# Kernel optimization log

Measured on AMD Instinct MI355X. Metric: run time of the kernel, lower is better.

Reference implementation:

```python
import jax, jax.numpy as jnp
import numpy as np


def _hard_sigmoid(x):
    # Keras ConvLSTM2D default recurrent_activation
    return jnp.clip(0.2 * x + 0.5, 0.0, 1.0)


def _conv(x, w):
    # NHWC input, HWIO kernel, SAME padding, stride 1
    return jax.lax.conv_general_dilated(
        x, w, (1, 1), 'SAME', dimension_numbers=('NHWC', 'HWIO', 'NHWC'))


def _convlstm(seq, h, c, k, rk, b):
    # seq: [B, T, H, W, Cin]; h, c: [B, H, W, F]
    # k: [kh, kw, Cin, 4F], rk: [kh, kw, F, 4F], b: [4F]
    def step(carry, x):
        h, c = carry
        z = _conv(x, k) + _conv(h, rk) + b  # [B,H,W,4F]
        zi, zf, zc, zo = jnp.split(z, 4, axis=-1)
        i = _hard_sigmoid(zi)
        f = _hard_sigmoid(zf)
        o = _hard_sigmoid(zo)
        c = f * c + i * jnp.tanh(zc)
        h = o * jnp.tanh(c)
        return (h, c), None
    (h, c), _ = jax.lax.scan(step, (h, c), jnp.swapaxes(seq, 0, 1))
    return h, c


def setup_inputs() -> dict:
    key = jax.random.key(0)
    ks = jax.random.split(key, 14)
    B, T, H, W, Cin, F, K = 32, 1, 64, 64, 1, 64, 3
    s = 0.05
    inp = {
        'input_': jax.random.normal(ks[0], (B, T, H, W, Cin), jnp.float32),
        'h0': jax.random.normal(ks[1], (B, H, W, F), jnp.float32) * s,
        'c0': jax.random.normal(ks[2], (B, H, W, F), jnp.float32) * s,
        'h1': jax.random.normal(ks[3], (B, H, W, F), jnp.float32) * s,
        'c1': jax.random.normal(ks[4], (B, H, W, F), jnp.float32) * s,
        'k0': jax.random.normal(ks[5], (K, K, Cin, 4 * F), jnp.float32) * s,
        'rk0': jax.random.normal(ks[6], (K, K, F, 4 * F), jnp.float32) * s,
        'b0': jnp.zeros((4 * F,), jnp.float32),
        'k1': jax.random.normal(ks[7], (K, K, F, 4 * F), jnp.float32) * s,
        'rk1': jax.random.normal(ks[8], (K, K, F, 4 * F), jnp.float32) * s,
        'b1': jnp.zeros((4 * F,), jnp.float32),
        'cw': jax.random.normal(ks[9], (1, 1, F, 1), jnp.float32) * s,
        'cb': jnp.zeros((1,), jnp.float32),
    }
    return inp


def reference(input_, h0, c0, h1, c1, k0, rk0, b0, k1, rk1, b1, cw, cb):
    # Layer 0 consumes the input frame sequence (T=1)
    h0n, c0n = _convlstm(input_, h0, c0, k0, rk0, b0)
    # Layer 1 consumes layer-0's last hidden state as its (length-1) input
    h1n, c1n = _convlstm(h0n[:, None], h1, c1, k1, rk1, b1)
    frames = _conv(h1n, cw) + cb  # 1x1 conv head -> [B,H,W,1]
    return frames, h0n, c0n, h1n, c1n
```

## Files before the change

kernel.cpp:

```cpp
#include <hip/hip_runtime.h>
#include <hip/hip_bf16.h>

typedef short s16;
typedef __attribute__((ext_vector_type(8))) short bf16x8;
typedef __attribute__((ext_vector_type(4))) float f32x4;

__device__ __forceinline__ s16 f2bf(float f) {
  unsigned u = __builtin_bit_cast(unsigned, f);
  unsigned r = (u + 0x7FFFu + ((u >> 16) & 1u)) >> 16;
  return (s16)r;
}

__device__ __forceinline__ float hsig(float x) {
  return fminf(fmaxf(0.2f * x + 0.5f, 0.0f), 1.0f);
}

#define PXS 66
#define ROWSZ (PXS * 64)
#define ASZ4 (4 * ROWSZ)
#define ASZ6 (6 * ROWSZ)

__global__ void wprep_kernel(const float* __restrict__ rk0, const float* __restrict__ k1,
                             const float* __restrict__ rk1, const float* __restrict__ k0,
                             s16* __restrict__ w0q, s16* __restrict__ w1q,
                             s16* __restrict__ w2q, s16* __restrict__ k0t) {
  int idx = blockIdx.x * 256 + threadIdx.x;
  const int n1 = 18 * 8192;
  if (idx < 3 * n1) {
    int which = idx / n1;
    int i = idx - which * n1;
    int e    = i & 7;
    int lane = (i >> 3) & 63;
    int g    = (i >> 9) & 3;
    int j    = (i >> 11) & 3;
    int k    = (i >> 13) & 1;
    int tap  = i >> 14;
    int l15 = lane & 15, l4 = lane >> 4;
    int ic = k * 32 + l4 * 8 + e;
    int oc = j * 64 + g * 16 + l15;
    const float* src = (which == 0) ? rk0 : (which == 1) ? k1 : rk1;
    s16* dst = (which == 0) ? w0q : (which == 1) ? w1q : w2q;
    dst[i] = f2bf(src[(tap * 64 + ic) * 256 + oc]);
  } else if (idx < 3 * n1 + 8192) {
    int r = idx - 3 * n1;
    int kk = r & 31;
    int oc = r >> 5;
    k0t[r] = (kk < 9) ? f2bf(k0[kk * 256 + oc]) : (s16)0;
  }
}

template <bool F32>
__device__ __forceinline__ bf16x8 load_conv8(const void* src, long off) {
  if constexpr (F32) {
    const float* p = (const float*)src + off;
    float4 v0 = *reinterpret_cast<const float4*>(p);
    float4 v1 = *reinterpret_cast<const float4*>(p + 4);
    bf16x8 r;
    r[0] = f2bf(v0.x); r[1] = f2bf(v0.y); r[2] = f2bf(v0.z); r[3] = f2bf(v0.w);
    r[4] = f2bf(v1.x); r[5] = f2bf(v1.y); r[6] = f2bf(v1.z); r[7] = f2bf(v1.w);
    return r;
  } else {
    return *reinterpret_cast<const bf16x8*>((const s16*)src + off);
  }
}

template <bool F32, int ROWS, int NT>
__device__ __forceinline__ void stageA(s16* a_lds, const void* src, int b, int y0, int tid) {
  #pragma unroll
  for (int i = 0; i < ROWS * 512 / NT; ++i) {
    int c   = tid + i * NT;
    int row = c >> 9;
    int px  = (c >> 3) & 63;
    int cb  = c & 7;
    int y   = y0 - 1 + row;
    int xp  = px + 1;
    bf16x8 v = {};
    if ((unsigned)y < 64u)
      v = load_conv8<F32>(src, ((long)(b * 64 + y) * 64 + px) * 64 + cb * 8);
    *reinterpret_cast<bf16x8*>(a_lds + (row * PXS + xp) * 64 + ((cb ^ (xp & 7)) * 8)) = v;
  }
  if (tid < ROWS * 16) {
    int row = tid >> 4;
    int xp  = ((tid >> 3) & 1) ? 65 : 0;
    int cb  = tid & 7;
    bf16x8 z = {};
    *reinterpret_cast<bf16x8*>(a_lds + (row * PXS + xp) * 64 + cb * 8) = z;
  }
}

__global__ __launch_bounds__(1024, 1) void cell0_kernel(
    const float* __restrict__ h0,
    const s16* __restrict__ w0,
    const float* __restrict__ xin,
    const s16* __restrict__ k0t,
    const float* __restrict__ bias,
    const float* __restrict__ c_old,
    float* __restrict__ h_out,
    float* __restrict__ c_out,
    s16* __restrict__ hb_out)
{
  __shared__ __align__(16) s16 a_lds[ASZ6];
  __shared__ __align__(16) s16 w_lds[3][8192];
  __shared__ float x_lds[384];

  const int tid = threadIdx.x;
  const int b  = blockIdx.x >> 4;
  const int y0 = (blockIdx.x & 15) << 2;

  const int wave = tid >> 6;
  const int lane = tid & 63;
  const int g    = wave & 3;
  const int mh   = wave >> 2;
  const int l15  = lane & 15;
  const int l4   = lane >> 4;

  constexpr int NST = 18;

  auto issueW = [&](int u) {
    int v = (u >= NST) ? u - NST : u;
    const s16* wt = w0 + v * 8192;
    char* base = (char*)(&w_lds[0][0]) + (v % 3) * 16384 + (tid >> 6) * 1024;
    __builtin_amdgcn_global_load_lds(
        (const __attribute__((address_space(1))) void*)(wt + tid * 8),
        (__attribute__((address_space(3))) void*)base, 16, 0, 0);
  };
  auto readWf = [&](bf16x8 (&wf)[4], int slot) {
    const s16* wb = &w_lds[slot][0] + g * 512 + lane * 8;
    #pragma unroll
    for (int j = 0; j < 4; ++j)
      wf[j] = *reinterpret_cast<const bf16x8*>(wb + j * 2048);
  };

  f32x4 acc[4][4] = {};

  auto doStage = [&](const bf16x8 (&wf)[4], int u) {
    int tap = u >> 1, kk = u & 1;
    int dy = tap / 3, dx = tap - dy * 3;
    const char* sb = (const char*)a_lds + (mh + dy) * (ROWSZ * 2);
    bf16x8 af[4];
    #pragma unroll
    for (int m = 0; m < 4; ++m) {
      int xq   = m * 16 + l15 + dx;
      int boff = xq * 128 + ((((kk << 2) | l4) ^ (xq & 7)) << 4);
      af[m] = *reinterpret_cast<const bf16x8*>(sb + boff);
    }
    __builtin_amdgcn_s_setprio(1);
    #pragma unroll
    for (int m = 0; m < 4; ++m) {
      #pragma unroll
      for (int j = 0; j < 4; ++j)
        acc[m][j] = __builtin_amdgcn_mfma_f32_16x16x32_bf16(af[m], wf[j], acc[m][j], 0, 0, 0);
    }
    __builtin_amdgcn_s_setprio(0);
  };

  issueW(0);
  issueW(1);
  stageA<true, 6, 1024>(a_lds, h0, b, y0, tid);
  if (tid < 384) {
    int row = tid >> 6, px = tid & 63;
    int y = y0 - 1 + row;
    x_lds[tid] = ((unsigned)y < 64u) ? xin[(b * 64 + y) * 64 + px] : 0.0f;
  }
  __syncthreads();

  {
    bf16x8 bx[4];
    #pragma unroll
    for (int j = 0; j < 4; ++j) {
      int oc = j * 64 + g * 16 + l15;
      bx[j] = *reinterpret_cast<const bf16x8*>(k0t + oc * 32 + l4 * 8);
    }
    #pragma unroll
    for (int m = 0; m < 4; ++m) {
      int px = m * 16 + l15;
      bf16x8 ax = {};
      #pragma unroll
      for (int e = 0; e < 8; ++e) {
        int t = l4 * 8 + e;
        if (t < 9) {
          int dyt = t / 3, dxt = t - dyt * 3;
          int xx = px + dxt - 1;
          float xv = ((unsigned)xx < 64u) ? x_lds[(mh + dyt) * 64 + xx] : 0.0f;
          ax[e] = f2bf(xv);
        }
      }
      #pragma unroll
      for (int j = 0; j < 4; ++j)
        acc[m][j] = __builtin_amdgcn_mfma_f32_16x16x32_bf16(ax, bx[j], acc[m][j], 0, 0, 0);
    }
  }

  bf16x8 wf[4];
  #pragma unroll
  for (int u = 0; u < NST; ++u) {
    asm volatile("s_waitcnt vmcnt(1)" ::: "memory");
    __builtin_amdgcn_s_barrier();
    __builtin_amdgcn_sched_barrier(0);
    issueW(u + 2);
    readWf(wf, u % 3);
    doStage(wf, u);
  }

  float bi[4];
  #pragma unroll
  for (int j = 0; j < 4; ++j) bi[j] = bias[j * 64 + g * 16 + l15];
  const int pix_base = b * 4096 + y0 * 64;
  const int f = g * 16 + l15;
  #pragma unroll
  for (int m = 0; m < 4; ++m) {
    #pragma unroll
    for (int r = 0; r < 4; ++r) {
      int pl = mh * 64 + m * 16 + l4 * 4 + r;
      int off = (pix_base + pl) * 64 + f;
      float zi = acc[m][0][r] + bi[0];
      float zf = acc[m][1][r] + bi[1];
      float zc = acc[m][2][r] + bi[2];
      float zo = acc[m][3][r] + bi[3];
      float ig = hsig(zi), fg = hsig(zf), og = hsig(zo);
      float cn = fg * c_old[off] + ig * tanhf(zc);
      float hn = og * tanhf(cn);
      c_out[off] = cn;
      h_out[off] = hn;
      hb_out[off] = f2bf(hn);
    }
  }
}

__global__ __launch_bounds__(1024, 4) void cell1_kernel(
    const s16* __restrict__ src0,
    const float* __restrict__ src1,
    const s16* __restrict__ w0,
    const s16* __restrict__ w1,
    const float* __restrict__ bias,
    const float* __restrict__ c_old,
    float* __restrict__ h_out,
    float* __restrict__ c_out)
{
  __shared__ __align__(16) s16 a_lds[2 * ASZ4];
  __shared__ __align__(16) s16 w_lds[4][8192];

  const int tid = threadIdx.x;
  const int b  = blockIdx.x >> 5;
  const int y0 = (blockIdx.x & 31) << 1;

  const int wave = tid >> 6;
  const int lane = tid & 63;
  const int g    = wave & 3;
  const int mq   = wave >> 2;
  const int l15  = lane & 15;
  const int l4   = lane >> 4;

  constexpr int NST = 36;

  auto issueW = [&](int u) {
    int v = (u >= NST) ? u - NST : u;
    int si = (v >= 18) ? 1 : 0;
    const s16* wt = (si ? w1 : w0) + (v - 18 * si) * 8192;
    char* base = (char*)(&w_lds[0][0]) + (u & 3) * 16384 + (tid >> 6) * 1024;
    __builtin_amdgcn_global_load_lds(
        (const __attribute__((address_space(1))) void*)(wt + tid * 8),
        (__attribute__((address_space(3))) void*)base, 16, 0, 0);
  };

  auto readWf = [&](bf16x8 (&wf)[4], int u) {
    const s16* wb = &w_lds[u & 3][0] + g * 512 + lane * 8;
    #pragma unroll
    for (int j = 0; j < 4; ++j)
      wf[j] = *reinterpret_cast<const bf16x8*>(wb + j * 2048);
  };

  auto readA = [&](bf16x8 (&af)[2], int u) {
    int v = (u >= NST) ? u - NST : u;
    int si = (v >= 18) ? 1 : 0;
    int uu = v - 18 * si;
    int tap = uu >> 1, kk = uu & 1;
    int dy = tap / 3, dx = tap - dy * 3;
    const char* sb = (const char*)a_lds + si * (ASZ4 * 2) + ((mq >> 1) + dy) * (ROWSZ * 2);
    #pragma unroll
    for (int m = 0; m < 2; ++m) {
      int xq   = (mq & 1) * 32 + m * 16 + l15 + dx;
      int boff = xq * 128 + ((((kk << 2) | l4) ^ (xq & 7)) << 4);
      af[m] = *reinterpret_cast<const bf16x8*>(sb + boff);
    }
  };

  f32x4 acc[2][4] = {};

  auto doMfma = [&](const bf16x8 (&af)[2], const bf16x8 (&wf)[4]) {
    __builtin_amdgcn_s_setprio(1);
    #pragma unroll
    for (int m = 0; m < 2; ++m) {
      #pragma unroll
      for (int j = 0; j < 4; ++j)
        acc[m][j] = __builtin_amdgcn_mfma_f32_16x16x32_bf16(af[m], wf[j], acc[m][j], 0, 0, 0);
    }
    __builtin_amdgcn_s_setprio(0);
  };

  issueW(0);
  issueW(1);
  issueW(2);
  stageA<false, 4, 1024>(a_lds, src0, b, y0, tid);
  stageA<true, 4, 1024>(a_lds + ASZ4, src1, b, y0, tid);
  __syncthreads();

  bf16x8 afA[2], afB[2], wfA[4], wfB[4];
  readA(afA, 0);
  readWf(wfA, 0);
  #pragma unroll
  for (int u = 0; u < NST; u += 2) {
    asm volatile("s_waitcnt vmcnt(1)" ::: "memory");
    __builtin_amdgcn_s_barrier();
    issueW(u + 3);
    readA(afB, u + 1);
    readWf(wfB, u + 1);
    doMfma(afA, wfA);
    asm volatile("s_waitcnt vmcnt(1)" ::: "memory");
    __builtin_amdgcn_s_barrier();
    issueW(u + 4);
    readA(afA, u + 2);
    readWf(wfA, u + 2);
    doMfma(afB, wfB);
  }

  float bi[4];
  #pragma unroll
  for (int j = 0; j < 4; ++j) bi[j] = bias[j * 64 + g * 16 + l15];
  const int pix_base = b * 4096 + y0 * 64;
  const int f = g * 16 + l15;
  #pragma unroll
  for (int m = 0; m < 2; ++m) {
    #pragma unroll
    for (int r = 0; r < 4; ++r) {
      int pl = mq * 32 + m * 16 + l4 * 4 + r;
      int off = (pix_base + pl) * 64 + f;
      float zi = acc[m][0][r] + bi[0];
      float zf = acc[m][1][r] + bi[1];
      float zc = acc[m][2][r] + bi[2];
      float zo = acc[m][3][r] + bi[3];
      float ig = hsig(zi), fg = hsig(zf), og = hsig(zo);
      float cn = fg * c_old[off] + ig * tanhf(zc);
      float hn = og * tanhf(cn);
      c_out[off] = cn;
      h_out[off] = hn;
    }
  }
}

__global__ void frames_kernel(const float* __restrict__ h, const float* __restrict__ cw,
                              const float* __restrict__ cbp, float* __restrict__ out) {
  int tid = blockIdx.x * 256 + threadIdx.x;
  int p  = tid >> 2;
  int fc = (tid & 3) * 16;
  const float4* hp = reinterpret_cast<const float4*>(h + p * 64 + fc);
  const float4* wp = reinterpret_cast<const float4*>(cw + fc);
  float s = 0.0f;
  #pragma unroll
  for (int i = 0; i < 4; ++i) {
    float4 v = hp[i];
    float4 w = wp[i];
    s += v.x * w.x + v.y * w.y + v.z * w.z + v.w * w.w;
  }
  s += __shfl_xor(s, 1);
  s += __shfl_xor(s, 2);
  if ((tid & 3) == 0) out[p] = s + cbp[0];
}

extern "C" void kernel_launch(void* const* d_in, const int* in_sizes, int n_in,
                              void* d_out, int out_size, void* d_ws, size_t ws_size,
                              hipStream_t stream) {
  const float* x   = (const float*)d_in[0];
  const float* h0  = (const float*)d_in[1];
  const float* c0  = (const float*)d_in[2];
  const float* h1  = (const float*)d_in[3];
  const float* c1  = (const float*)d_in[4];
  const float* k0  = (const float*)d_in[5];
  const float* rk0 = (const float*)d_in[6];
  const float* b0  = (const float*)d_in[7];
  const float* k1  = (const float*)d_in[8];
  const float* rk1 = (const float*)d_in[9];
  const float* b1  = (const float*)d_in[10];
  const float* cw  = (const float*)d_in[11];
  const float* cbp = (const float*)d_in[12];

  float* out    = (float*)d_out;
  float* frames = out;
  float* h0n    = out + 131072;
  float* c0n    = out + 131072 + 8388608;
  float* h1n    = out + 131072 + 2 * 8388608;
  float* c1n    = out + 131072 + 3 * 8388608;

  char* ws = (char*)d_ws;
  const size_t SZ_H = 16777216;
  s16* h0nb = (s16*)(ws + 0 * SZ_H);
  s16* w0q  = (s16*)(ws + 1 * SZ_H);
  s16* w1q  = (s16*)(ws + 1 * SZ_H + 1 * 294912);
  s16* w2q  = (s16*)(ws + 1 * SZ_H + 2 * 294912);
  s16* k0t  = (s16*)(ws + 1 * SZ_H + 3 * 294912);

  wprep_kernel<<<1760, 256, 0, stream>>>(rk0, k1, rk1, k0, w0q, w1q, w2q, k0t);

  cell0_kernel<<<512, 1024, 0, stream>>>(
      h0, w0q, x, k0t, b0, c0, h0n, c0n, h0nb);

  cell1_kernel<<<1024, 1024, 0, stream>>>(
      h0nb, h1, w1q, w2q, b1, c1, h1n, c1n);

  frames_kernel<<<2048, 256, 0, stream>>>(h1n, cw, cbp, frames);
}
```

Before: 182.2 us.

## Hold cell1 weights in registers and transpose gates through LDS for vector epilogue

Cell1 drops from 1024 to 512 threads and stops streaming weight slices through a 4-deep LDS ring buffer. Each wave now loads its 18 weight fragments per source straight into registers and loops over 8 pixel tiles, so every weight fragment is reused across more pixels. The per-step barriers and async global-to-LDS copies go away. The epilogue writes gate pre-activations to LDS, reads them back transposed, and does float4 loads and stores for c/h. The cost is heavy register pressure (36 bf16x8 weight registers plus 16 accumulators), which risks spills and lower occupancy. Weights are also reloaded from global per block with no overlap against the compute.

```diff
diff --git a/kernel.cpp b/kernel.cpp
--- a/kernel.cpp
+++ b/kernel.cpp
@@ -227,7 +227,8 @@
   }
 }
 
-__global__ __launch_bounds__(1024, 4) void cell1_kernel(
+#define ZP 260
+__global__ __launch_bounds__(512, 2) void cell1_kernel(
     const s16* __restrict__ src0,
     const float* __restrict__ src1,
     const s16* __restrict__ w0,
@@ -238,7 +239,6 @@
     float* __restrict__ c_out)
 {
   __shared__ __align__(16) s16 a_lds[2 * ASZ4];
-  __shared__ __align__(16) s16 w_lds[4][8192];
 
   const int tid = threadIdx.x;
   const int b  = blockIdx.x >> 5;
@@ -246,104 +246,113 @@
 
   const int wave = tid >> 6;
   const int lane = tid & 63;
-  const int g    = wave & 3;
-  const int mq   = wave >> 2;
+  const int j    = wave & 3;
+  const int fh   = wave >> 2;
   const int l15  = lane & 15;
   const int l4   = lane >> 4;
 
-  constexpr int NST = 36;
-
-  auto issueW = [&](int u) {
-    int v = (u >= NST) ? u - NST : u;
-    int si = (v >= 18) ? 1 : 0;
-    const s16* wt = (si ? w1 : w0) + (v - 18 * si) * 8192;
-    char* base = (char*)(&w_lds[0][0]) + (u & 3) * 16384 + (tid >> 6) * 1024;
-    __builtin_amdgcn_global_load_lds(
-        (const __attribute__((address_space(1))) void*)(wt + tid * 8),
-        (__attribute__((address_space(3))) void*)base, 16, 0, 0);
-  };
-
-  auto readWf = [&](bf16x8 (&wf)[4], int u) {
-    const s16* wb = &w_lds[u & 3][0] + g * 512 + lane * 8;
-    #pragma unroll
-    for (int j = 0; j < 4; ++j)
-      wf[j] = *reinterpret_cast<const bf16x8*>(wb + j * 2048);
-  };
-
-  auto readA = [&](bf16x8 (&af)[2], int u) {
-    int v = (u >= NST) ? u - NST : u;
-    int si = (v >= 18) ? 1 : 0;
-    int uu = v - 18 * si;
-    int tap = uu >> 1, kk = uu & 1;
+  bf16x8 wreg[18][2];
+  {
+    const s16* wb = w0 + j * 2048 + fh * 1024 + lane * 8;
+    #pragma unroll
+    for (int u = 0; u < 18; ++u) {
+      wreg[u][0] = *reinterpret_cast<const bf16x8*>(wb + u * 8192);
+      wreg[u][1] = *reinterpret_cast<const bf16x8*>(wb + u * 8192 + 512);
+    }
+  }
+
+  stageA<false, 4, 512>(a_lds, src0, b, y0, tid);
+  stageA<true, 4, 512>(a_lds + ASZ4, src1, b, y0, tid);
+  __syncthreads();
+
+  f32x4 acc[8][2] = {};
+
+  #pragma unroll
+  for (int u = 0; u < 18; ++u) {
+    int tap = u >> 1, kk = u & 1;
     int dy = tap / 3, dx = tap - dy * 3;
-    const char* sb = (const char*)a_lds + si * (ASZ4 * 2) + ((mq >> 1) + dy) * (ROWSZ * 2);
-    #pragma unroll
-    for (int m = 0; m < 2; ++m) {
-      int xq   = (mq & 1) * 32 + m * 16 + l15 + dx;
+    #pragma unroll
+    for (int m = 0; m < 8; ++m) {
+      int row  = (m >> 2) + dy;
+      int xq   = (m & 3) * 16 + l15 + dx;
       int boff = xq * 128 + ((((kk << 2) | l4) ^ (xq & 7)) << 4);
-      af[m] = *reinterpret_cast<const bf16x8*>(sb + boff);
-    }
-  };
-
-  f32x4 acc[2][4] = {};
-
-  auto doMfma = [&](const bf16x8 (&af)[2], const bf16x8 (&wf)[4]) {
-    __builtin_amdgcn_s_setprio(1);
-    #pragma unroll
-    for (int m = 0; m < 2; ++m) {
+      bf16x8 a = *reinterpret_cast<const bf16x8*>((const char*)a_lds + row * (ROWSZ * 2) + boff);
+      acc[m][0] = __builtin_amdgcn_mfma_f32_16x16x32_bf16(a, wreg[u][0], acc[m][0], 0, 0, 0);
+      acc[m][1] = __builtin_amdgcn_mfma_f32_16x16x32_bf16(a, wreg[u][1], acc[m][1], 0, 0, 0);
+    }
+  }
+
+  {
+    const s16* wb = w1 + j * 2048 + fh * 1024 + lane * 8;
+    #pragma unroll
+    for (int u = 0; u < 18; ++u) {
+      wreg[u][0] = *reinterpret_cast<const bf16x8*>(wb + u * 8192);
+      wreg[u][1] = *reinterpret_cast<const bf16x8*>(wb + u * 8192 + 512);
+    }
+  }
+
+  #pragma unroll
+  for (int u = 0; u < 18; ++u) {
+    int tap = u >> 1, kk = u & 1;
+    int dy = tap / 3, dx = tap - dy * 3;
+    #pragma unroll
+    for (int m = 0; m < 8; ++m) {
+      int row  = (m >> 2) + dy;
+      int xq   = (m & 3) * 16 + l15 + dx;
+      int boff = xq * 128 + ((((kk << 2) | l4) ^ (xq & 7)) << 4);
+      bf16x8 a = *reinterpret_cast<const bf16x8*>((const char*)a_lds + ASZ4 * 2 + row * (ROWSZ * 2) + boff);
+      acc[m][0] = __builtin_amdgcn_mfma_f32_16x16x32_bf16(a, wreg[u][0], acc[m][0], 0, 0, 0);
+      acc[m][1] = __builtin_amdgcn_mfma_f32_16x16x32_bf16(a, wreg[u][1], acc[m][1], 0, 0, 0);
+    }
+  }
+
+  float* z_lds = (float*)a_lds;
+  const int pix_base = b * 4096 + y0 * 64;
+  #pragma unroll
+  for (int h = 0; h < 2; ++h) {
+    __syncthreads();
+    #pragma unroll
+    for (int mm = 0; mm < 4; ++mm) {
       #pragma unroll
-      for (int j = 0; j < 4; ++j)
-        acc[m][j] = __builtin_amdgcn_mfma_f32_16x16x32_bf16(af[m], wf[j], acc[m][j], 0, 0, 0);
-    }
-    __builtin_amdgcn_s_setprio(0);
-  };
-
-  issueW(0);
-  issueW(1);
-  issueW(2);
-  stageA<false, 4, 1024>(a_lds, src0, b, y0, tid);
-  stageA<true, 4, 1024>(a_lds + ASZ4, src1, b, y0, tid);
-  __syncthreads();
-
-  bf16x8 afA[2], afB[2], wfA[4], wfB[4];
-  readA(afA, 0);
-  readWf(wfA, 0);
-  #pragma unroll
-  for (int u = 0; u < NST; u += 2) {
-    asm volatile("s_waitcnt vmcnt(1)" ::: "memory");
-    __builtin_amdgcn_s_barrier();
-    issueW(u + 3);
-    readA(afB, u + 1);
-    readWf(wfB, u + 1);
-    doMfma(afA, wfA);
-    asm volatile("s_waitcnt vmcnt(1)" ::: "memory");
-    __builtin_amdgcn_s_barrier();
-    issueW(u + 4);
-    readA(afA, u + 2);
-    readWf(wfA, u + 2);
-    doMfma(afB, wfB);
-  }
-
-  float bi[4];
-  #pragma unroll
-  for (int j = 0; j < 4; ++j) bi[j] = bias[j * 64 + g * 16 + l15];
-  const int pix_base = b * 4096 + y0 * 64;
-  const int f = g * 16 + l15;
-  #pragma unroll
-  for (int m = 0; m < 2; ++m) {
-    #pragma unroll
-    for (int r = 0; r < 4; ++r) {
-      int pl = mq * 32 + m * 16 + l4 * 4 + r;
-      int off = (pix_base + pl) * 64 + f;
-      float zi = acc[m][0][r] + bi[0];
-      float zf = acc[m][1][r] + bi[1];
-      float zc = acc[m][2][r] + bi[2];
-      float zo = acc[m][3][r] + bi[3];
-      float ig = hsig(zi), fg = hsig(zf), og = hsig(zo);
-      float cn = fg * c_old[off] + ig * tanhf(zc);
-      float hn = og * tanhf(cn);
-      c_out[off] = cn;
-      h_out[off] = hn;
+      for (int q = 0; q < 2; ++q) {
+        int oc = j * 64 + fh * 32 + q * 16 + l15;
+        #pragma unroll
+        for (int r = 0; r < 4; ++r) {
+          int px = mm * 16 + l4 * 4 + r;
+          z_lds[px * ZP + oc] = acc[h * 4 + mm][q][r];
+        }
+      }
+    }
+    __syncthreads();
+    int px8 = wave * 8 + (lane >> 3);
+    int f0  = (lane & 7) * 8;
+    const float* zr = z_lds + px8 * ZP;
+    int off0 = (pix_base + h * 64 + px8) * 64 + f0;
+    #pragma unroll
+    for (int half8 = 0; half8 < 2; ++half8) {
+      float4 zi4 = *reinterpret_cast<const float4*>(zr + f0 + half8 * 4);
+      float4 zf4 = *reinterpret_cast<const float4*>(zr + 64 + f0 + half8 * 4);
+      float4 zc4 = *reinterpret_cast<const float4*>(zr + 128 + f0 + half8 * 4);
+      float4 zo4 = *reinterpret_cast<const float4*>(zr + 192 + f0 + half8 * 4);
+      float4 bi4 = *reinterpret_cast<const float4*>(bias + f0 + half8 * 4);
+      float4 bf4 = *reinterpret_cast<const float4*>(bias + 64 + f0 + half8 * 4);
+      float4 bc4 = *reinterpret_cast<const float4*>(bias + 128 + f0 + half8 * 4);
+      float4 bo4 = *reinterpret_cast<const float4*>(bias + 192 + f0 + half8 * 4);
+      float4 co4 = *reinterpret_cast<const float4*>(c_old + off0 + half8 * 4);
+      float4 hn4, cn4;
+      #pragma unroll
+      for (int e = 0; e < 4; ++e) {
+        float zi = (&zi4.x)[e] + (&bi4.x)[e];
+        float zf = (&zf4.x)[e] + (&bf4.x)[e];
+        float zc = (&zc4.x)[e] + (&bc4.x)[e];
+        float zo = (&zo4.x)[e] + (&bo4.x)[e];
+        float ig = hsig(zi), fg = hsig(zf), og = hsig(zo);
+        float cn = fg * (&co4.x)[e] + ig * tanhf(zc);
+        (&cn4.x)[e] = cn;
+        (&hn4.x)[e] = og * tanhf(cn);
+      }
+      *reinterpret_cast<float4*>(c_out + off0 + half8 * 4) = cn4;
+      *reinterpret_cast<float4*>(h_out + off0 + half8 * 4) = hn4;
     }
   }
 }
@@ -404,7 +413,7 @@
   cell0_kernel<<<512, 1024, 0, stream>>>(
       h0, w0q, x, k0t, b0, c0, h0n, c0n, h0nb);
 
-  cell1_kernel<<<1024, 1024, 0, stream>>>(
+  cell1_kernel<<<1024, 512, 0, stream>>>(
       h0nb, h1, w1q, w2q, b1, c1, h1n, c1n);
 
   frames_kernel<<<2048, 256, 0, stream>>>(h1n, cw, cbp, frames);
```

New measurement: 208.3 us. 1.14x slower.
